# Kernel optimization log

Measured on AMD Instinct MI355X. Metric: run time of the kernel, lower is better.

## Reference

```python
import jax, jax.numpy as jnp
import numpy as np

EPSILON = 0.3
ALPHA = 0.7
LN_EPS = 1e-5


def _layernorm(x, g, b):
    mu = jnp.mean(x, axis=-1, keepdims=True)
    var = jnp.mean((x - mu) ** 2, axis=-1, keepdims=True)
    return (x - mu) / jnp.sqrt(var + LN_EPS) * g + b


def setup_inputs() -> dict:
    key = jax.random.key(0)
    ks = jax.random.split(key, 6)
    B, N, D, L = 1, 2048, 768, 16
    s = 0.05  # weight scale to keep sigmoid/exp well-conditioned
    return {
        "x": jax.random.normal(ks[0], (B, N, D), jnp.float32),
        "proj_w": jax.random.normal(ks[1], (D, L), jnp.float32) * s,
        "proj_b": jnp.zeros((L,), jnp.float32),
        "ln1_g": jnp.ones((L,), jnp.float32),
        "ln1_b": jnp.zeros((L,), jnp.float32),
        "pi_w1": jax.random.normal(ks[2], (L, D), jnp.float32) * s,
        "pi_b1": jnp.zeros((D,), jnp.float32),
        "pi_w2": jax.random.normal(ks[3], (D, 1), jnp.float32) * s,
        "pi_b2": jnp.zeros((1,), jnp.float32),
        "dt": jnp.full((1,), 0.05, jnp.float32),
        "f_w": jax.random.normal(ks[4], (D, D), jnp.float32) * s,
        "f_b": jnp.zeros((D,), jnp.float32),
        "ln2_g": jnp.ones((D,), jnp.float32),
        "ln2_b": jnp.zeros((D,), jnp.float32),
    }


def reference(x, proj_w, proj_b, ln1_g, ln1_b, pi_w1, pi_b1, pi_w2, pi_b2, dt, f_w, f_b, ln2_g, ln2_b):
    B, N, D = x.shape
    # proj_list: Linear -> LayerNorm -> ReLU. [B,N,L]
    x_proj = jax.nn.relu(_layernorm(x @ proj_w + proj_b, ln1_g, ln1_b))
    # RBF kernel over pairwise differences. [B,N,N]
    diff = x_proj[:, :, None, :] - x_proj[:, None, :, :]
    K_eps = jnp.exp(-(1.0 / (4.0 * EPSILON)) * jnp.sum(diff * diff, axis=-1))
    q_tilde = jnp.sum(K_eps, axis=2)  # [B,N]
    # pi_list: Linear -> ReLU -> Linear -> Sigmoid. [B,N]
    pi = jax.nn.sigmoid(jax.nn.relu(x_proj @ pi_w1 + pi_b1) @ pi_w2 + pi_b2)[..., 0]
    v = pi / q_tilde  # diagonal of D_epsilon_tilde
    # K_tilde = K_eps @ diag(v): column scaling (math-equivalent to bmm with diag_embed)
    K_tilde = K_eps * v[:, None, :]
    d = jnp.sum(K_tilde, axis=2) + 1e-5  # diagonal of D_tilde
    # inv(D_tilde) @ K_tilde: row scaling; then subtract identity
    L_op = (1.0 / EPSILON) * (K_tilde / d[:, :, None]) - jnp.eye(N, dtype=x.dtype)[None]
    L_mat = L_op[0]  # .squeeze(0), B == 1
    # f(x): modeled as linear map
    target = x @ f_w + f_b  # [B,N,D]
    tt = dt * jnp.einsum('ij,bjd->bid', L_mat, target)  # target_transformed
    target1 = target + tt
    target2 = ALPHA * x + (1.0 - ALPHA) * (target1 + tt)
    return _layernorm(target2, ln2_g, ln2_b)
```

## Files before the change

kernel.cpp:

```cpp
#include <hip/hip_runtime.h>
#include <math.h>

#define EPSILON 0.3f
#define ALPHA 0.7f
#define LN_EPS 1e-5f

typedef __bf16 bf16x8 __attribute__((ext_vector_type(8)));
typedef float f32x4 __attribute__((ext_vector_type(4)));

__device__ __forceinline__ unsigned short f2bf(float f) {
  unsigned int u = __float_as_uint(f);
  return (unsigned short)((u + 0x7fffu + ((u >> 16) & 1u)) >> 16);
}
__device__ __forceinline__ unsigned int pack2(float lo, float hi) {
  return (unsigned int)f2bf(lo) | ((unsigned int)f2bf(hi) << 16);
}

__device__ __forceinline__ void async16(const unsigned short* g,
                                        unsigned short* l) {
  __builtin_amdgcn_global_load_lds(
      (const __attribute__((address_space(1))) unsigned int*)g,
      (__attribute__((address_space(3))) unsigned int*)l, 16, 0, 0);
}

__device__ __forceinline__ float wave_reduce(float v) {
#pragma unroll
  for (int off = 32; off > 0; off >>= 1) v += __shfl_xor(v, off, 64);
  return v;
}

__device__ __forceinline__ float blk_reduce_sum(float v, float* red) {
  v = wave_reduce(v);
  int lane = threadIdx.x & 63, wid = threadIdx.x >> 6;
  __syncthreads();
  if (lane == 0) red[wid] = v;
  __syncthreads();
  return red[0] + red[1] + red[2] + red[3];
}

__device__ __forceinline__ void gridbar(int* base, int nBlk, int bid) {
  __syncthreads();
  if (threadIdx.x == 0) {
    __threadfence();
    __hip_atomic_fetch_add(base + (bid & 7) * 32, 1, __ATOMIC_RELAXED,
                           __HIP_MEMORY_SCOPE_AGENT);
    int iters = 0;
    for (;;) {
      int sum = 0;
#pragma unroll
      for (int i = 0; i < 8; ++i)
        sum += __hip_atomic_load(base + i * 32, __ATOMIC_RELAXED,
                                 __HIP_MEMORY_SCOPE_AGENT);
      if (sum >= nBlk) break;
      __builtin_amdgcn_s_sleep(4);
      if (++iters > (1 << 20)) break;
    }
    __threadfence();
  }
  __syncthreads();
}

struct ProjSh {
  float xs[16][68];
  float ws[64][20];
  float ysh[16][17];
  float xps[16][16];
  float pr[16][4];
};

__global__ __launch_bounds__(256) void k_mega2(
    const float* __restrict__ x, const float* __restrict__ proj_w,
    const float* __restrict__ proj_b, const float* __restrict__ ln1_g,
    const float* __restrict__ ln1_b, const float* __restrict__ pi_w1,
    const float* __restrict__ pi_b1, const float* __restrict__ pi_w2,
    const float* __restrict__ pi_b2, const float* __restrict__ dtp,
    const float* __restrict__ fw, const float* __restrict__ fb,
    const float* __restrict__ ln2_g, const float* __restrict__ ln2_b,
    unsigned short* __restrict__ Kb, unsigned short* __restrict__ xvbT,
    unsigned short* __restrict__ fwTb, unsigned short* __restrict__ Z,
    float* __restrict__ xp, float* __restrict__ s, float* __restrict__ pi,
    float* __restrict__ v, float* __restrict__ dv, float* __restrict__ out,
    int* __restrict__ bar, int N, int D) {
  __shared__ __align__(16) unsigned char pool[32768];
  __shared__ float qs[4][4];
  const int tid = threadIdx.x;
  const int bid = blockIdx.x;
  const int nBlk = gridDim.x;
  const int lane = tid & 63, wv = tid >> 6;

  {
    int nProj = N / 16;
    int cols = D / 64;
    int nItems = nProj + cols * cols;
    for (int item = bid; item < nItems; item += nBlk) {
      __syncthreads();
      if (item >= nProj) {
        int t = item - nProj;
        unsigned short(*tile)[65] = (unsigned short(*)[65])pool;
        int c0 = (t % cols) * 64, r0 = (t / cols) * 64;
#pragma unroll
        for (int i = 0; i < 16; ++i) {
          int rr = wv * 16 + i;
          tile[rr][lane] = f2bf(fw[(size_t)(r0 + rr) * D + c0 + lane]);
        }
        __syncthreads();
#pragma unroll
        for (int i = 0; i < 16; ++i) {
          int rr = wv * 16 + i;
          fwTb[(size_t)(c0 + rr) * D + r0 + lane] = tile[lane][rr];
        }
        continue;
      }
      ProjSh& P = *(ProjSh*)pool;
      int row0 = item * 16;
      int row = tid >> 4, l = tid & 15;
      int skc = (tid & 15) * 4;
      int wk = tid >> 2, wl = (tid & 3) * 4;
      float acc = 0.f;
      for (int k0 = 0; k0 < D; k0 += 64) {
        float4 xv = *(const float4*)(x + (size_t)(row0 + row) * D + k0 + skc);
        float4 wvec = *(const float4*)(proj_w + (size_t)(k0 + wk) * 16 + wl);
        __syncthreads();
        *(float4*)&P.xs[row][skc] = xv;
        *(float4*)&P.ws[wk][wl] = wvec;
        __syncthreads();
#pragma unroll
        for (int kk = 0; kk < 64; kk += 4) {
          float4 a4 = *(const float4*)&P.xs[row][kk];
          acc += a4.x * P.ws[kk + 0][l];
          acc += a4.y * P.ws[kk + 1][l];
          acc += a4.z * P.ws[kk + 2][l];
          acc += a4.w * P.ws[kk + 3][l];
        }
      }
      float y = acc + proj_b[l];
      P.ysh[row][l] = y;
      __syncthreads();
      float mu = 0.f;
#pragma unroll
      for (int t = 0; t < 16; ++t) mu += P.ysh[row][t];
      mu *= (1.f / 16.f);
      float var = 0.f;
#pragma unroll
      for (int t = 0; t < 16; ++t) {
        float d2 = P.ysh[row][t] - mu;
        var += d2 * d2;
      }
      var *= (1.f / 16.f);
      float rstd = rsqrtf(var + LN_EPS);
      float xpv = fmaxf((y - mu) * rstd * ln1_g[l] + ln1_b[l], 0.f);
      P.xps[row][l] = xpv;
      xp[(size_t)(row0 + row) * 16 + l] = xpv;
      float sq = xpv * xpv;
      sq += __shfl_xor(sq, 8, 64);
      sq += __shfl_xor(sq, 4, 64);
      sq += __shfl_xor(sq, 2, 64);
      sq += __shfl_xor(sq, 1, 64);
      if ((lane & 15) == 0) s[row0 + row] = sq;
      __syncthreads();
      float w1r[3][16], b1r[3], w2r[3];
#pragma unroll
      for (int c = 0; c < 3; ++c) {
        int d0 = tid + c * 256;
        b1r[c] = pi_b1[d0];
        w2r[c] = pi_w2[d0];
#pragma unroll
        for (int t = 0; t < 16; ++t) w1r[c][t] = pi_w1[(size_t)t * D + d0];
      }
#pragma unroll
      for (int r = 0; r < 16; ++r) {
        float xv2[16];
#pragma unroll
        for (int t4 = 0; t4 < 4; ++t4) {
          float4 xq = *(const float4*)&P.xps[r][t4 * 4];
          xv2[t4 * 4 + 0] = xq.x;
          xv2[t4 * 4 + 1] = xq.y;
          xv2[t4 * 4 + 2] = xq.z;
          xv2[t4 * 4 + 3] = xq.w;
        }
        float pa = 0.f;
#pragma unroll
        for (int c = 0; c < 3; ++c) {
          float h = b1r[c];
#pragma unroll
          for (int t = 0; t < 16; ++t) h += xv2[t] * w1r[c][t];
          h = fmaxf(h, 0.f);
          pa += h * w2r[c];
        }
        float pv = wave_reduce(pa);
        if (lane == 0) P.pr[r][wv] = pv;
      }
      __syncthreads();
      if (tid < 16) {
        float tot = P.pr[tid][0] + P.pr[tid][1] + P.pr[tid][2] + P.pr[tid][3] +
                    pi_b2[0];
        pi[row0 + tid] = 1.f / (1.f + expf(-tot));
      }
    }
  }
  gridbar(bar + 0 * 256, nBlk, bid);

  {
    int nItems = N / 4;
    for (int item = bid; item < nItems; item += nBlk) {
      __syncthreads();
      int i0 = item * 4;
      float a[4][16], si[4];
#pragma unroll
      for (int r = 0; r < 4; ++r) {
        const float* ap = xp + (size_t)(i0 + r) * 16;
#pragma unroll
        for (int t = 0; t < 16; ++t) a[r][t] = ap[t];
        si[r] = s[i0 + r];
      }
      const float cc = 1.f / (4.f * EPSILON);
      float qa[4] = {0.f, 0.f, 0.f, 0.f};
      for (int it = 0; it < N / 512; ++it) {
        int j = it * 512 + tid * 2;
        const float4* bp = (const float4*)(xp + (size_t)j * 16);
        float4 b0 = bp[0], b1 = bp[1], b2 = bp[2], b3 = bp[3];
        float4 c0 = bp[4], c1 = bp[5], c2 = bp[6], c3 = bp[7];
        float bvv[16] = {b0.x, b0.y, b0.z, b0.w, b1.x, b1.y, b1.z, b1.w,
                         b2.x, b2.y, b2.z, b2.w, b3.x, b3.y, b3.z, b3.w};
        float cvv[16] = {c0.x, c0.y, c0.z, c0.w, c1.x, c1.y, c1.z, c1.w,
                         c2.x, c2.y, c2.z, c2.w, c3.x, c3.y, c3.z, c3.w};
        float sj0 = s[j], sj1 = s[j + 1];
#pragma unroll
        for (int r = 0; r < 4; ++r) {
          float d0 = 0.f, d1 = 0.f;
#pragma unroll
          for (int t = 0; t < 16; ++t) {
            d0 += a[r][t] * bvv[t];
            d1 += a[r][t] * cvv[t];
          }
          float k0 = __expf(-cc * (si[r] + sj0 - 2.f * d0));
          float k1 = __expf(-cc * (si[r] + sj1 - 2.f * d1));
          *(unsigned int*)(Kb + (size_t)(i0 + r) * N + j) = pack2(k0, k1);
          qa[r] += k0 + k1;
        }
      }
#pragma unroll
      for (int r = 0; r < 4; ++r) {
        float t = wave_reduce(qa[r]);
        if (lane == 0) qs[r][wv] = t;
      }
      __syncthreads();
      if (tid < 4) {
        float tot = qs[tid][0] + qs[tid][1] + qs[tid][2] + qs[tid][3];
        v[i0 + tid] = pi[i0 + tid] / tot;
      }
    }
  }
  gridbar(bar + 1 * 256, nBlk, bid);

  {
    int nDv = N / 4;
    int cols = D / 64;
    int nXT = cols * (N / 64);
    for (int item = bid; item < nDv + nXT; item += nBlk) {
      if (item < nDv) {
        int i = item * 4 + wv;
        const unsigned short* kr = Kb + (size_t)i * N;
        float acc = 0.f;
        for (int c0 = lane * 8; c0 < N; c0 += 512) {
          uint4 kv = *(const uint4*)(kr + c0);
          float4 va = *(const float4*)(v + c0);
          float4 vb = *(const float4*)(v + c0 + 4);
          unsigned int u;
          u = kv.x;
          acc += __uint_as_float(u << 16) * va.x +
                 __uint_as_float(u & 0xffff0000u) * va.y;
          u = kv.y;
          acc += __uint_as_float(u << 16) * va.z +
                 __uint_as_float(u & 0xffff0000u) * va.w;
          u = kv.z;
          acc += __uint_as_float(u << 16) * vb.x +
                 __uint_as_float(u & 0xffff0000u) * vb.y;
          u = kv.w;
          acc += __uint_as_float(u << 16) * vb.z +
                 __uint_as_float(u & 0xffff0000u) * vb.w;
        }
        acc = wave_reduce(acc);
        if (lane == 0) dv[i] = acc + 1e-5f;
      } else {
        int t = item - nDv;
        __syncthreads();
        unsigned short(*tile)[65] = (unsigned short(*)[65])pool;
        int c0 = (t % cols) * 64, r0 = (t / cols) * 64;
#pragma unroll
        for (int i = 0; i < 16; ++i) {
          int rr = wv * 16 + i;
          tile[rr][lane] =
              f2bf(v[r0 + rr] * x[(size_t)(r0 + rr) * D + c0 + lane]);
        }
        __syncthreads();
#pragma unroll
        for (int i = 0; i < 16; ++i) {
          int rr = wv * 16 + i;
          xvbT[(size_t)(c0 + rr) * N + r0 + lane] = tile[lane][rr];
        }
      }
    }
  }
  gridbar(bar + 2 * 256, nBlk, bid);

  {
    float dtv = dtp[0];
    float c2 = (1.f - ALPHA) * (1.f - 2.f * dtv);
    float c3b = (1.f - ALPHA) * 2.f * dtv / EPSILON;
    unsigned short* As = (unsigned short*)pool;
    unsigned short* Bs = As + 64 * 128;
    int tilesX = D / 64;
    int nT = tilesX * (N / 64);
    int ln = lane & 15, quad = lane >> 4;
    int mh = (wv & 1) * 32, nh = (wv >> 1) * 32;
    int srow = wv * 4 + quad;
    int swz = (ln ^ srow) * 8;
    for (int item = bid; item < nT; item += nBlk) {
      int row0 = (item / tilesX) * 64, col0 = (item % tilesX) * 64;
      const unsigned short* gA = Kb + (size_t)(row0 + srow) * N + swz;
      const unsigned short* gB = xvbT + (size_t)(col0 + srow) * N + swz;
      f32x4 acc[2][2] = {};
      for (int k0 = 0; k0 < N; k0 += 128) {
        __syncthreads();
#pragma unroll
        for (int q = 0; q < 4; ++q) {
          async16(gA + (size_t)q * 16 * N + k0, As + (q * 16 + wv * 4) * 128);
          async16(gB + (size_t)q * 16 * N + k0, Bs + (q * 16 + wv * 4) * 128);
        }
        __syncthreads();
#pragma unroll
        for (int ks = 0; ks < 4; ++ks) {
          bf16x8 bfr[2], afr[2];
#pragma unroll
          for (int nt = 0; nt < 2; ++nt) {
            int r = nh + nt * 16 + ln;
            int cix = (ks * 4 + quad) ^ (r & 15);
            bfr[nt] = *(const bf16x8*)&Bs[r * 128 + cix * 8];
          }
#pragma unroll
          for (int mt = 0; mt < 2; ++mt) {
            int r = mh + mt * 16 + ln;
            int cix = (ks * 4 + quad) ^ (r & 15);
            afr[mt] = *(const bf16x8*)&As[r * 128 + cix * 8];
          }
#pragma unroll
          for (int mt = 0; mt < 2; ++mt)
#pragma unroll
            for (int nt = 0; nt < 2; ++nt)
              acc[mt][nt] = __builtin_amdgcn_mfma_f32_16x16x32_bf16(
                  afr[mt], bfr[nt], acc[mt][nt], 0, 0, 0);
        }
      }
#pragma unroll
      for (int mt = 0; mt < 2; ++mt)
#pragma unroll
        for (int nt = 0; nt < 2; ++nt) {
          int col = col0 + nh + nt * 16 + ln;
#pragma unroll
          for (int r = 0; r < 4; ++r) {
            int row = row0 + mh + mt * 16 + quad * 4 + r;
            float c3 = c3b / dv[row];
            Z[(size_t)row * D + col] =
                f2bf(c2 * x[(size_t)row * D + col] + c3 * acc[mt][nt][r]);
          }
        }
    }
  }
  gridbar(bar + 3 * 256, nBlk, bid);

  {
    float dtv = dtp[0];
    float cb = (1.f - ALPHA) * (1.f - 2.f * dtv) +
               (1.f - ALPHA) * 2.f * dtv / EPSILON;
    unsigned short* As = (unsigned short*)pool;
    unsigned short* Bs = As + 64 * 128;
    int tilesX = D / 64;
    int nT = tilesX * (N / 64);
    int ln = lane & 15, quad = lane >> 4;
    int mh = (wv & 1) * 32, nh = (wv >> 1) * 32;
    int srow = wv * 4 + quad;
    int swz = (ln ^ srow) * 8;
    for (int item = bid; item < nT; item += nBlk) {
      int row0 = (item / tilesX) * 64, col0 = (item % tilesX) * 64;
      const unsigned short* gA = Z + (size_t)(row0 + srow) * D + swz;
      const unsigned short* gB = fwTb + (size_t)(col0 + srow) * D + swz;
      f32x4 acc[2][2] = {};
      for (int k0 = 0; k0 < D; k0 += 128) {
        __syncthreads();
#pragma unroll
        for (int q = 0; q < 4; ++q) {
          async16(gA + (size_t)q * 16 * D + k0, As + (q * 16 + wv * 4) * 128);
          async16(gB + (size_t)q * 16 * D + k0, Bs + (q * 16 + wv * 4) * 128);
        }
        __syncthreads();
#pragma unroll
        for (int ks = 0; ks < 4; ++ks) {
          bf16x8 bfr[2], afr[2];
#pragma unroll
          for (int nt = 0; nt < 2; ++nt) {
            int r = nh + nt * 16 + ln;
            int cix = (ks * 4 + quad) ^ (r & 15);
            bfr[nt] = *(const bf16x8*)&Bs[r * 128 + cix * 8];
          }
#pragma unroll
          for (int mt = 0; mt < 2; ++mt) {
            int r = mh + mt * 16 + ln;
            int cix = (ks * 4 + quad) ^ (r & 15);
            afr[mt] = *(const bf16x8*)&As[r * 128 + cix * 8];
          }
#pragma unroll
          for (int mt = 0; mt < 2; ++mt)
#pragma unroll
            for (int nt = 0; nt < 2; ++nt)
              acc[mt][nt] = __builtin_amdgcn_mfma_f32_16x16x32_bf16(
                  afr[mt], bfr[nt], acc[mt][nt], 0, 0, 0);
        }
      }
#pragma unroll
      for (int mt = 0; mt < 2; ++mt)
#pragma unroll
        for (int nt = 0; nt < 2; ++nt) {
          int col = col0 + nh + nt * 16 + ln;
          float bv = cb * fb[col];
#pragma unroll
          for (int r = 0; r < 4; ++r) {
            int row = row0 + mh + mt * 16 + quad * 4 + r;
            size_t idx = (size_t)row * D + col;
            out[idx] = ALPHA * x[idx] + acc[mt][nt][r] + bv;
          }
        }
    }
  }
  gridbar(bar + 4 * 256, nBlk, bid);

  {
    int nItems = N / 4;
    for (int item = bid; item < nItems; item += nBlk) {
      int i = item * 4 + wv;
      float4 vv[3];
      float sum = 0.f;
#pragma unroll
      for (int t = 0; t < 3; ++t) {
        vv[t] = *(const float4*)(out + (size_t)i * D + lane * 4 + t * 256);
        sum += vv[t].x + vv[t].y + vv[t].z + vv[t].w;
      }
      float mu = wave_reduce(sum) / (float)D;
      float sq = 0.f;
#pragma unroll
      for (int t = 0; t < 3; ++t) {
        float dx = vv[t].x - mu, dy = vv[t].y - mu;
        float dz = vv[t].z - mu, dw = vv[t].w - mu;
        sq += dx * dx + dy * dy + dz * dz + dw * dw;
      }
      float var = wave_reduce(sq) / (float)D;
      float rs = rsqrtf(var + LN_EPS);
#pragma unroll
      for (int t = 0; t < 3; ++t) {
        int d0 = lane * 4 + t * 256;
        float4 gv = *(const float4*)(ln2_g + d0);
        float4 bv = *(const float4*)(ln2_b + d0);
        float4 o;
        o.x = (vv[t].x - mu) * rs * gv.x + bv.x;
        o.y = (vv[t].y - mu) * rs * gv.y + bv.y;
        o.z = (vv[t].z - mu) * rs * gv.z + bv.z;
        o.w = (vv[t].w - mu) * rs * gv.w + bv.w;
        *(float4*)(out + (size_t)i * D + d0) = o;
      }
    }
  }
}


__global__ __launch_bounds__(256) void k_proj(
    const float* __restrict__ x, const float* __restrict__ proj_w,
    const float* __restrict__ proj_b, const float* __restrict__ ln1_g,
    const float* __restrict__ ln1_b, const float* __restrict__ pi_w1,
    const float* __restrict__ pi_b1, const float* __restrict__ pi_w2,
    const float* __restrict__ pi_b2, const float* __restrict__ fw,
    unsigned short* __restrict__ fwTb, float* __restrict__ xp,
    float* __restrict__ s, float* __restrict__ pi, int N, int D) {
  __shared__ float xs[16][68];
  __shared__ float ws[64][20];
  __shared__ float ysh[16][17];
  __shared__ float xps[16][16];
  __shared__ float pr[16][4];
  int tid = threadIdx.x;
  int nProj = N / 16;
  if (blockIdx.x >= (unsigned)nProj) {
    unsigned short(*tile)[33] = (unsigned short(*)[33])&ws[0][0];
    int t = blockIdx.x - nProj;
    int tx = tid & 31, ty = tid >> 5;
    int cols = D / 32;
    int c0 = (t % cols) * 32, r0 = (t / cols) * 32;
#pragma unroll
    for (int i = 0; i < 4; ++i) {
      int r = r0 + ty + i * 8;
      tile[ty + i * 8][tx] = f2bf(fw[(size_t)r * D + c0 + tx]);
    }
    __syncthreads();
#pragma unroll
    for (int i = 0; i < 4; ++i) {
      int cc = c0 + ty + i * 8;
      fwTb[(size_t)cc * D + r0 + tx] = tile[tx][ty + i * 8];
    }
    return;
  }
  int row0 = blockIdx.x * 16;
  int row = tid >> 4, l = tid & 15;
  int lane = tid & 63, w = tid >> 6;
  int skc = (tid & 15) * 4;
  int wk = tid >> 2, wl = (tid & 3) * 4;
  float acc = 0.f;
  for (int k0 = 0; k0 < D; k0 += 64) {
    float4 xv = *(const float4*)(x + (size_t)(row0 + row) * D + k0 + skc);
    float4 wv = *(const float4*)(proj_w + (size_t)(k0 + wk) * 16 + wl);
    __syncthreads();
    *(float4*)&xs[row][skc] = xv;
    *(float4*)&ws[wk][wl] = wv;
    __syncthreads();
#pragma unroll
    for (int kk = 0; kk < 64; kk += 4) {
      float4 a4 = *(const float4*)&xs[row][kk];
      acc += a4.x * ws[kk + 0][l];
      acc += a4.y * ws[kk + 1][l];
      acc += a4.z * ws[kk + 2][l];
      acc += a4.w * ws[kk + 3][l];
    }
  }
  float y = acc + proj_b[l];
  ysh[row][l] = y;
  __syncthreads();
  float mu = 0.f;
#pragma unroll
  for (int t = 0; t < 16; ++t) mu += ysh[row][t];
  mu *= (1.f / 16.f);
  float var = 0.f;
#pragma unroll
  for (int t = 0; t < 16; ++t) { float d2 = ysh[row][t] - mu; var += d2 * d2; }
  var *= (1.f / 16.f);
  float rstd = rsqrtf(var + LN_EPS);
  float xpv = fmaxf((y - mu) * rstd * ln1_g[l] + ln1_b[l], 0.f);
  xps[row][l] = xpv;
  xp[(size_t)(row0 + row) * 16 + l] = xpv;
  float sq = xpv * xpv;
  sq += __shfl_xor(sq, 8, 64);
  sq += __shfl_xor(sq, 4, 64);
  sq += __shfl_xor(sq, 2, 64);
  sq += __shfl_xor(sq, 1, 64);
  if ((lane & 15) == 0) s[row0 + row] = sq;
  __syncthreads();
  float w1r[3][16], b1r[3], w2r[3];
#pragma unroll
  for (int c = 0; c < 3; ++c) {
    int d0 = tid + c * 256;
    b1r[c] = pi_b1[d0];
    w2r[c] = pi_w2[d0];
#pragma unroll
    for (int t = 0; t < 16; ++t) w1r[c][t] = pi_w1[(size_t)t * D + d0];
  }
#pragma unroll
  for (int r = 0; r < 16; ++r) {
    float xv[16];
#pragma unroll
    for (int t4 = 0; t4 < 4; ++t4) {
      float4 xq = *(const float4*)&xps[r][t4 * 4];
      xv[t4 * 4 + 0] = xq.x; xv[t4 * 4 + 1] = xq.y;
      xv[t4 * 4 + 2] = xq.z; xv[t4 * 4 + 3] = xq.w;
    }
    float pa = 0.f;
#pragma unroll
    for (int c = 0; c < 3; ++c) {
      float h = b1r[c];
#pragma unroll
      for (int t = 0; t < 16; ++t) h += xv[t] * w1r[c][t];
      h = fmaxf(h, 0.f);
      pa += h * w2r[c];
    }
    float pv = wave_reduce(pa);
    if (lane == 0) pr[r][w] = pv;
  }
  __syncthreads();
  if (tid < 16) {
    float tot = pr[tid][0] + pr[tid][1] + pr[tid][2] + pr[tid][3] + pi_b2[0];
    pi[row0 + tid] = 1.f / (1.f + expf(-tot));
  }
}

__global__ __launch_bounds__(256) void k_keps(
    const float* __restrict__ xp, const float* __restrict__ s,
    const float* __restrict__ pi, unsigned short* __restrict__ Kb,
    float* __restrict__ v, int N) {
  __shared__ float qs[4][4];
  int i0 = blockIdx.x * 4;
  int tid = threadIdx.x, lane = tid & 63, w = tid >> 6;
  float a[4][16], si[4];
#pragma unroll
  for (int r = 0; r < 4; ++r) {
    const float* ap = xp + (size_t)(i0 + r) * 16;
#pragma unroll
    for (int t = 0; t < 16; ++t) a[r][t] = ap[t];
    si[r] = s[i0 + r];
  }
  const float c = 1.f / (4.f * EPSILON);
  float qa[4] = {0.f, 0.f, 0.f, 0.f};
  for (int it = 0; it < N / 512; ++it) {
    int j = it * 512 + tid * 2;
    const float4* bp = (const float4*)(xp + (size_t)j * 16);
    float4 b0 = bp[0], b1 = bp[1], b2 = bp[2], b3 = bp[3];
    float4 c0 = bp[4], c1 = bp[5], c2 = bp[6], c3 = bp[7];
    float bv[16] = {b0.x, b0.y, b0.z, b0.w, b1.x, b1.y, b1.z, b1.w,
                    b2.x, b2.y, b2.z, b2.w, b3.x, b3.y, b3.z, b3.w};
    float cv[16] = {c0.x, c0.y, c0.z, c0.w, c1.x, c1.y, c1.z, c1.w,
                    c2.x, c2.y, c2.z, c2.w, c3.x, c3.y, c3.z, c3.w};
    float sj0 = s[j], sj1 = s[j + 1];
#pragma unroll
    for (int r = 0; r < 4; ++r) {
      float d0 = 0.f, d1 = 0.f;
#pragma unroll
      for (int t = 0; t < 16; ++t) { d0 += a[r][t] * bv[t]; d1 += a[r][t] * cv[t]; }
      float k0 = __expf(-c * (si[r] + sj0 - 2.f * d0));
      float k1 = __expf(-c * (si[r] + sj1 - 2.f * d1));
      *(unsigned int*)(Kb + (size_t)(i0 + r) * N + j) = pack2(k0, k1);
      qa[r] += k0 + k1;
    }
  }
#pragma unroll
  for (int r = 0; r < 4; ++r) {
    float t = wave_reduce(qa[r]);
    if (lane == 0) qs[r][w] = t;
  }
  __syncthreads();
  if (tid < 4) {
    float tot = qs[tid][0] + qs[tid][1] + qs[tid][2] + qs[tid][3];
    v[i0 + tid] = pi[i0 + tid] / tot;
  }
}

__global__ __launch_bounds__(256) void k_prep(
    const unsigned short* __restrict__ Kb, const float* __restrict__ v,
    float* __restrict__ dv, const float* __restrict__ x,
    unsigned short* __restrict__ xvbT, int N, int D) {
  __shared__ float sh[544];
  int bid = blockIdx.x, tid = threadIdx.x;
  if (bid < N) {
    int i = bid;
    float acc = 0.f;
    for (int j8 = tid * 8; j8 < N; j8 += 256 * 8) {
      uint4 kv4 = *(const uint4*)(Kb + (size_t)i * N + j8);
      float4 va = *(const float4*)(v + j8);
      float4 vb = *(const float4*)(v + j8 + 4);
      unsigned int u;
      u = kv4.x;
      acc += __uint_as_float(u << 16) * va.x + __uint_as_float(u & 0xffff0000u) * va.y;
      u = kv4.y;
      acc += __uint_as_float(u << 16) * va.z + __uint_as_float(u & 0xffff0000u) * va.w;
      u = kv4.z;
      acc += __uint_as_float(u << 16) * vb.x + __uint_as_float(u & 0xffff0000u) * vb.y;
      u = kv4.w;
      acc += __uint_as_float(u << 16) * vb.z + __uint_as_float(u & 0xffff0000u) * vb.w;
    }
    float tot = blk_reduce_sum(acc, sh);
    if (tid == 0) dv[i] = tot + 1e-5f;
  } else {
    int t = bid - N;
    unsigned short(*tile)[33] = (unsigned short(*)[33])sh;
    int tx = tid & 31, ty = tid >> 5;
    int cols = D / 32;
    int c0 = (t % cols) * 32;
    int r0 = (t / cols) * 32;
#pragma unroll
    for (int i = 0; i < 4; ++i) {
      int r = r0 + ty + i * 8;
      tile[ty + i * 8][tx] = f2bf(v[r] * x[(size_t)r * D + c0 + tx]);
    }
    __syncthreads();
#pragma unroll
    for (int i = 0; i < 4; ++i) {
      int cc = c0 + ty + i * 8;
      xvbT[(size_t)cc * N + r0 + tx] = tile[tx][ty + i * 8];
    }
  }
}

#define GEMM_KLOOP(Aptr, Bptr, Kdim)                                          \
  int tid = threadIdx.x;                                                      \
  int w = tid >> 6, l = tid & 63;                                             \
  int ln = l & 15, quad = l >> 4;                                             \
  int mh = (w & 1) * 32, nh = (w >> 1) * 32;                                  \
  int row0 = blockIdx.y * 64, col0 = blockIdx.x * 64;                         \
  int srow = w * 4 + (l >> 4);                                                \
  int swz = ((l & 15) ^ srow) * 8;                                            \
  const unsigned short* gA = Aptr + (size_t)(row0 + srow) * Kdim + swz;       \
  const unsigned short* gB = Bptr + (size_t)(col0 + srow) * Kdim + swz;       \
  f32x4 acc[2][2] = {};                                                       \
  for (int k0 = 0; k0 < Kdim; k0 += 128) {                                    \
    __syncthreads();                                                          \
    _Pragma("unroll")                                                         \
    for (int q = 0; q < 4; ++q) {                                             \
      async16(gA + (size_t)q * 16 * Kdim + k0, As + (q * 16 + w * 4) * 128);  \
      async16(gB + (size_t)q * 16 * Kdim + k0, Bs + (q * 16 + w * 4) * 128);  \
    }                                                                         \
    __syncthreads();                                                          \
    _Pragma("unroll")                                                         \
    for (int ks = 0; ks < 4; ++ks) {                                          \
      bf16x8 bfr[2], afr[2];                                                  \
      _Pragma("unroll")                                                       \
      for (int nt = 0; nt < 2; ++nt) {                                        \
        int r = nh + nt * 16 + ln;                                            \
        int cix = (ks * 4 + quad) ^ (r & 15);                                 \
        bfr[nt] = *(const bf16x8*)&Bs[r * 128 + cix * 8];                     \
      }                                                                       \
      _Pragma("unroll")                                                       \
      for (int mt = 0; mt < 2; ++mt) {                                        \
        int r = mh + mt * 16 + ln;                                            \
        int cix = (ks * 4 + quad) ^ (r & 15);                                 \
        afr[mt] = *(const bf16x8*)&As[r * 128 + cix * 8];                     \
      }                                                                       \
      _Pragma("unroll")                                                       \
      for (int mt = 0; mt < 2; ++mt)                                          \
        _Pragma("unroll")                                                     \
        for (int nt = 0; nt < 2; ++nt)                                        \
          acc[mt][nt] = __builtin_amdgcn_mfma_f32_16x16x32_bf16(              \
              afr[mt], bfr[nt], acc[mt][nt], 0, 0, 0);                        \
    }                                                                         \
  }

__global__ __launch_bounds__(256) void k_gemmA(
    const unsigned short* __restrict__ A, const unsigned short* __restrict__ Bt,
    const float* __restrict__ x, const float* __restrict__ dv,
    const float* __restrict__ dtp, unsigned short* __restrict__ Z,
    int M, int N, int K) {
  __shared__ unsigned short As[64 * 128];
  __shared__ unsigned short Bs[64 * 128];
  GEMM_KLOOP(A, Bt, K)
  float dtv = dtp[0];
  float c2 = (1.f - ALPHA) * (1.f - 2.f * dtv);
  float c3b = (1.f - ALPHA) * 2.f * dtv / EPSILON;
#pragma unroll
  for (int mt = 0; mt < 2; ++mt)
#pragma unroll
    for (int nt = 0; nt < 2; ++nt) {
      int col = col0 + nh + nt * 16 + ln;
#pragma unroll
      for (int r = 0; r < 4; ++r) {
        int row = row0 + mh + mt * 16 + quad * 4 + r;
        float c3 = c3b / dv[row];
        Z[(size_t)row * N + col] =
            f2bf(c2 * x[(size_t)row * N + col] + c3 * acc[mt][nt][r]);
      }
    }
}

__global__ __launch_bounds__(256) void k_gemmB(
    const unsigned short* __restrict__ A, const unsigned short* __restrict__ Bt,
    const float* __restrict__ x, const float* __restrict__ bias,
    const float* __restrict__ dtp, float* __restrict__ out,
    int M, int N, int K) {
  __shared__ unsigned short As[64 * 128];
  __shared__ unsigned short Bs[64 * 128];
  GEMM_KLOOP(A, Bt, K)
  float dtv = dtp[0];
  float cb = (1.f - ALPHA) * (1.f - 2.f * dtv) +
             (1.f - ALPHA) * 2.f * dtv / EPSILON;
#pragma unroll
  for (int mt = 0; mt < 2; ++mt)
#pragma unroll
    for (int nt = 0; nt < 2; ++nt) {
      int col = col0 + nh + nt * 16 + ln;
      float bv = cb * bias[col];
#pragma unroll
      for (int r = 0; r < 4; ++r) {
        int row = row0 + mh + mt * 16 + quad * 4 + r;
        size_t idx = (size_t)row * N + col;
        out[idx] = ALPHA * x[idx] + acc[mt][nt][r] + bv;
      }
    }
}

__global__ __launch_bounds__(256) void k_ln_rows(
    float* __restrict__ out, const float* __restrict__ g,
    const float* __restrict__ b, int D) {
  __shared__ float red[4];
  int i = blockIdx.x, tid = threadIdx.x;
  float vv[4];
  int nt = D / 256;
  float sum = 0.f;
  for (int t = 0; t < nt; ++t) {
    vv[t] = out[(size_t)i * D + tid + t * 256];
    sum += vv[t];
  }
  float mu = blk_reduce_sum(sum, red) / (float)D;
  float sq = 0.f;
  for (int t = 0; t < nt; ++t) { float d2 = vv[t] - mu; sq += d2 * d2; }
  float var = blk_reduce_sum(sq, red) / (float)D;
  float rs = rsqrtf(var + LN_EPS);
  for (int t = 0; t < nt; ++t) {
    int d0 = tid + t * 256;
    out[(size_t)i * D + d0] = (vv[t] - mu) * rs * g[d0] + b[d0];
  }
}

extern "C" void kernel_launch(void* const* d_in, const int* in_sizes, int n_in,
                              void* d_out, int out_size, void* d_ws, size_t ws_size,
                              hipStream_t stream) {
  const float* x = (const float*)d_in[0];
  const float* proj_w = (const float*)d_in[1];
  const float* proj_b = (const float*)d_in[2];
  const float* ln1_g = (const float*)d_in[3];
  const float* ln1_b = (const float*)d_in[4];
  const float* pi_w1 = (const float*)d_in[5];
  const float* pi_b1 = (const float*)d_in[6];
  const float* pi_w2 = (const float*)d_in[7];
  const float* pi_b2 = (const float*)d_in[8];
  const float* dt = (const float*)d_in[9];
  const float* f_w = (const float*)d_in[10];
  const float* f_b = (const float*)d_in[11];
  const float* ln2_g = (const float*)d_in[12];
  const float* ln2_b = (const float*)d_in[13];
  float* out = (float*)d_out;

  int D = in_sizes[11];
  int N = in_sizes[0] / D;

  unsigned short* Kb = (unsigned short*)d_ws;
  unsigned short* xvbT = Kb + (size_t)N * N;
  unsigned short* fwTb = xvbT + (size_t)D * N;
  unsigned short* Z = fwTb + (size_t)D * D;
  float* xp = (float*)(Z + (size_t)N * D);
  float* s = xp + (size_t)N * 16;
  float* pi = s + N;
  float* v = pi + N;
  float* dv = v + N;
  char* dvEnd = (char*)(dv + N);
  int* bar = (int*)((((uintptr_t)dvEnd) + 255) & ~(uintptr_t)255);

  bool ok = false;
  int maxBlk = 0;
  hipError_t qerr =
      hipOccupancyMaxActiveBlocksPerMultiprocessor(&maxBlk, k_mega2, 256, 0);
  if (qerr == hipSuccess && maxBlk > 0) {
    int dev = 0, numCU = 256;
    hipGetDevice(&dev);
    hipDeviceGetAttribute(&numCU, hipDeviceAttributeMultiprocessorCount, dev);
    long cap = (long)maxBlk * (long)numCU;
    int grid = (int)(cap < 512 ? cap : 512);
    if (grid >= 64) {
      hipMemsetAsync(bar, 0, 5 * 256 * sizeof(int), stream);
      k_mega2<<<grid, 256, 0, stream>>>(
          x, proj_w, proj_b, ln1_g, ln1_b, pi_w1, pi_b1, pi_w2, pi_b2, dt,
          f_w, f_b, ln2_g, ln2_b, Kb, xvbT, fwTb, Z, xp, s, pi, v, dv, out,
          bar, N, D);
      ok = true;
    }
  }

  if (!ok) {
    int fwB = (D / 32) * (D / 32);
    int xvtB = (D / 32) * (N / 32);
    k_proj<<<N / 16 + fwB, 256, 0, stream>>>(x, proj_w, proj_b, ln1_g, ln1_b,
                                             pi_w1, pi_b1, pi_w2, pi_b2, f_w,
                                             fwTb, xp, s, pi, N, D);
    k_keps<<<N / 4, 256, 0, stream>>>(xp, s, pi, Kb, v, N);
    k_prep<<<N + xvtB, 256, 0, stream>>>(Kb, v, dv, x, xvbT, N, D);
    k_gemmA<<<dim3(D / 64, N / 64), 256, 0, stream>>>(Kb, xvbT, x, dv, dt, Z,
                                                      N, D, N);
    k_gemmB<<<dim3(D / 64, N / 64), 256, 0, stream>>>(Z, fwTb, x, f_b, dt, out,
                                                      N, D, D);
    k_ln_rows<<<N, 256, 0, stream>>>(out, ln2_g, ln2_b, D);
  }
}
```

Measured before the change: 158.6 us.

## Double-buffer LDS tiles in both GEMM phases and remap tile order

Doubles the shared-memory pool so the two MFMA GEMM phases (K@xv and Z@fw^T) can prefetch the next 128-wide K slice into a second buffer while computing the current one. This removes one barrier per iteration and overlaps global-to-LDS loads with MFMA work. The tile-to-block assignment is also permuted into eight interleaved chunks to change locality across blocks. The larger LDS footprint can lower occupancy of the persistent mega-kernel. The async loads rely on a single trailing barrier for completion, which depends on the compiler inserting a vmcnt wait.

```diff
diff --git a/kernel.cpp b/kernel.cpp
--- a/kernel.cpp
+++ b/kernel.cpp
@@ -81,7 +81,7 @@
     float* __restrict__ xp, float* __restrict__ s, float* __restrict__ pi,
     float* __restrict__ v, float* __restrict__ dv, float* __restrict__ out,
     int* __restrict__ bar, int N, int D) {
-  __shared__ __align__(16) unsigned char pool[32768];
+  __shared__ __align__(16) unsigned char pool[65536];
   __shared__ float qs[4][4];
   const int tid = threadIdx.x;
   const int bid = blockIdx.x;
@@ -308,27 +308,45 @@
     float dtv = dtp[0];
     float c2 = (1.f - ALPHA) * (1.f - 2.f * dtv);
     float c3b = (1.f - ALPHA) * 2.f * dtv / EPSILON;
-    unsigned short* As = (unsigned short*)pool;
-    unsigned short* Bs = As + 64 * 128;
+    unsigned short* As0 = (unsigned short*)pool;
+    unsigned short* Bs0 = As0 + 64 * 128;
+    unsigned short* As1 = Bs0 + 64 * 128;
+    unsigned short* Bs1 = As1 + 64 * 128;
     int tilesX = D / 64;
     int nT = tilesX * (N / 64);
+    int qch = (nT + 7) >> 3;
     int ln = lane & 15, quad = lane >> 4;
     int mh = (wv & 1) * 32, nh = (wv >> 1) * 32;
     int srow = wv * 4 + quad;
     int swz = (ln ^ srow) * 8;
-    for (int item = bid; item < nT; item += nBlk) {
+    for (int raw = bid; raw < (qch << 3); raw += nBlk) {
+      int item = (raw & 7) * qch + (raw >> 3);
+      if (item >= nT) continue;
       int row0 = (item / tilesX) * 64, col0 = (item % tilesX) * 64;
       const unsigned short* gA = Kb + (size_t)(row0 + srow) * N + swz;
       const unsigned short* gB = xvbT + (size_t)(col0 + srow) * N + swz;
       f32x4 acc[2][2] = {};
+#pragma unroll
+      for (int q = 0; q < 4; ++q) {
+        async16(gA + (size_t)q * 16 * N, As0 + (q * 16 + wv * 4) * 128);
+        async16(gB + (size_t)q * 16 * N, Bs0 + (q * 16 + wv * 4) * 128);
+      }
+      __syncthreads();
+      int cur = 0;
       for (int k0 = 0; k0 < N; k0 += 128) {
-        __syncthreads();
-#pragma unroll
-        for (int q = 0; q < 4; ++q) {
-          async16(gA + (size_t)q * 16 * N + k0, As + (q * 16 + wv * 4) * 128);
-          async16(gB + (size_t)q * 16 * N + k0, Bs + (q * 16 + wv * 4) * 128);
-        }
-        __syncthreads();
+        unsigned short* Asc = cur ? As1 : As0;
+        unsigned short* Bsc = cur ? Bs1 : Bs0;
+        if (k0 + 128 < N) {
+          unsigned short* Asn = cur ? As0 : As1;
+          unsigned short* Bsn = cur ? Bs0 : Bs1;
+#pragma unroll
+          for (int q = 0; q < 4; ++q) {
+            async16(gA + (size_t)q * 16 * N + k0 + 128,
+                    Asn + (q * 16 + wv * 4) * 128);
+            async16(gB + (size_t)q * 16 * N + k0 + 128,
+                    Bsn + (q * 16 + wv * 4) * 128);
+          }
+        }
 #pragma unroll
         for (int ks = 0; ks < 4; ++ks) {
           bf16x8 bfr[2], afr[2];
@@ -336,13 +354,13 @@
           for (int nt = 0; nt < 2; ++nt) {
             int r = nh + nt * 16 + ln;
             int cix = (ks * 4 + quad) ^ (r & 15);
-            bfr[nt] = *(const bf16x8*)&Bs[r * 128 + cix * 8];
+            bfr[nt] = *(const bf16x8*)&Bsc[r * 128 + cix * 8];
           }
 #pragma unroll
           for (int mt = 0; mt < 2; ++mt) {
             int r = mh + mt * 16 + ln;
             int cix = (ks * 4 + quad) ^ (r & 15);
-            afr[mt] = *(const bf16x8*)&As[r * 128 + cix * 8];
+            afr[mt] = *(const bf16x8*)&Asc[r * 128 + cix * 8];
           }
 #pragma unroll
           for (int mt = 0; mt < 2; ++mt)
@@ -351,6 +369,8 @@
               acc[mt][nt] = __builtin_amdgcn_mfma_f32_16x16x32_bf16(
                   afr[mt], bfr[nt], acc[mt][nt], 0, 0, 0);
         }
+        __syncthreads();
+        cur ^= 1;
       }
 #pragma unroll
       for (int mt = 0; mt < 2; ++mt)
@@ -373,27 +393,45 @@
     float dtv = dtp[0];
     float cb = (1.f - ALPHA) * (1.f - 2.f * dtv) +
                (1.f - ALPHA) * 2.f * dtv / EPSILON;
-    unsigned short* As = (unsigned short*)pool;
-    unsigned short* Bs = As + 64 * 128;
+    unsigned short* As0 = (unsigned short*)pool;
+    unsigned short* Bs0 = As0 + 64 * 128;
+    unsigned short* As1 = Bs0 + 64 * 128;
+    unsigned short* Bs1 = As1 + 64 * 128;
     int tilesX = D / 64;
     int nT = tilesX * (N / 64);
+    int qch = (nT + 7) >> 3;
     int ln = lane & 15, quad = lane >> 4;
     int mh = (wv & 1) * 32, nh = (wv >> 1) * 32;
     int srow = wv * 4 + quad;
     int swz = (ln ^ srow) * 8;
-    for (int item = bid; item < nT; item += nBlk) {
+    for (int raw = bid; raw < (qch << 3); raw += nBlk) {
+      int item = (raw & 7) * qch + (raw >> 3);
+      if (item >= nT) continue;
       int row0 = (item / tilesX) * 64, col0 = (item % tilesX) * 64;
       const unsigned short* gA = Z + (size_t)(row0 + srow) * D + swz;
       const unsigned short* gB = fwTb + (size_t)(col0 + srow) * D + swz;
       f32x4 acc[2][2] = {};
+#pragma unroll
+      for (int q = 0; q < 4; ++q) {
+        async16(gA + (size_t)q * 16 * D, As0 + (q * 16 + wv * 4) * 128);
+        async16(gB + (size_t)q * 16 * D, Bs0 + (q * 16 + wv * 4) * 128);
+      }
+      __syncthreads();
+      int cur = 0;
       for (int k0 = 0; k0 < D; k0 += 128) {
-        __syncthreads();
-#pragma unroll
-        for (int q = 0; q < 4; ++q) {
-          async16(gA + (size_t)q * 16 * D + k0, As + (q * 16 + wv * 4) * 128);
-          async16(gB + (size_t)q * 16 * D + k0, Bs + (q * 16 + wv * 4) * 128);
-        }
-        __syncthreads();
+        unsigned short* Asc = cur ? As1 : As0;
+        unsigned short* Bsc = cur ? Bs1 : Bs0;
+        if (k0 + 128 < D) {
+          unsigned short* Asn = cur ? As0 : As1;
+          unsigned short* Bsn = cur ? Bs0 : Bs1;
+#pragma unroll
+          for (int q = 0; q < 4; ++q) {
+            async16(gA + (size_t)q * 16 * D + k0 + 128,
+                    Asn + (q * 16 + wv * 4) * 128);
+            async16(gB + (size_t)q * 16 * D + k0 + 128,
+                    Bsn + (q * 16 + wv * 4) * 128);
+          }
+        }
 #pragma unroll
         for (int ks = 0; ks < 4; ++ks) {
           bf16x8 bfr[2], afr[2];
@@ -401,13 +439,13 @@
           for (int nt = 0; nt < 2; ++nt) {
             int r = nh + nt * 16 + ln;
             int cix = (ks * 4 + quad) ^ (r & 15);
-            bfr[nt] = *(const bf16x8*)&Bs[r * 128 + cix * 8];
+            bfr[nt] = *(const bf16x8*)&Bsc[r * 128 + cix * 8];
           }
 #pragma unroll
           for (int mt = 0; mt < 2; ++mt) {
             int r = mh + mt * 16 + ln;
             int cix = (ks * 4 + quad) ^ (r & 15);
-            afr[mt] = *(const bf16x8*)&As[r * 128 + cix * 8];
+            afr[mt] = *(const bf16x8*)&Asc[r * 128 + cix * 8];
           }
 #pragma unroll
           for (int mt = 0; mt < 2; ++mt)
@@ -416,6 +454,8 @@
               acc[mt][nt] = __builtin_amdgcn_mfma_f32_16x16x32_bf16(
                   afr[mt], bfr[nt], acc[mt][nt], 0, 0, 0);
         }
+        __syncthreads();
+        cur ^= 1;
       }
 #pragma unroll
       for (int mt = 0; mt < 2; ++mt)
```

After: 157.6 us. About the same (-0.6%).
